# Optimization experiments

Measured on AMD Instinct MI355X. Metric: run time of the kernel, lower is better.

The kernel has to match this reference:

```python
import jax, jax.numpy as jnp
import numpy as np

HEADS = 8
DIM_HEAD = 64
CHUNK = 64        # seq chunk size
CCS = 128         # context chunk size
ALPHA = 32.0 ** 2 # stable-softmax alpha


def setup_inputs() -> dict:
    key = jax.random.key(0)
    ks = jax.random.split(key, 8)
    B, S, L, D = 4, 4097, 8065, 1024
    inner = HEADS * DIM_HEAD
    return dict(
        seq=jax.random.normal(ks[0], (B, S, D), jnp.float32),
        context=jax.random.normal(ks[1], (B, L, D), jnp.float32),
        Wq=jax.random.normal(ks[2], (D, inner), jnp.float32) * 0.02,
        Wkv=jax.random.normal(ks[3], (D, 2 * inner), jnp.float32) * 0.02,
        Wout=jax.random.normal(ks[4], (inner, D), jnp.float32) * 0.02,
        b_out=jnp.zeros((D,), jnp.float32),
        null_k=jax.random.normal(ks[5], (HEADS, DIM_HEAD), jnp.float32),
        null_v=jax.random.normal(ks[6], (HEADS, DIM_HEAD), jnp.float32),
        W_th=jax.random.normal(ks[7], (HEADS, HEADS), jnp.float32) * 0.2,
        b_th=jnp.zeros((HEADS,), jnp.float32),
    )


def reference(seq, context, Wq, Wkv, Wout, b_out, null_k, null_v, W_th, b_th):
    B, S, D = seq.shape
    # strip start tokens / pad to chunk multiples (matches torch F.pad logic)
    seq_len = S - 1                     # has_start_token -> seq_left_pad = -1
    ctx_len = context.shape[1] - 1      # context_has_start_token
    seq_rpad = (-seq_len) % CHUNK
    ctx_lpad = CCS - 1                  # context_left_pad = ccs - 1
    ctx_rpad = (-ctx_len) % CCS
    s = jnp.pad(seq[:, 1:], ((0, 0), (0, seq_rpad), (0, 0)))
    c = jnp.pad(context, ((0, 0), (ctx_lpad, ctx_rpad), (0, 0)))
    n = min(s.shape[1] // CHUNK, c.shape[1] // CCS)  # truncate to common chunks
    s = s[:, : n * CHUNK].reshape(B, n, CHUNK, D)
    c = c[:, : n * CCS].reshape(B, n, CCS, D)
    # projections -> b h n c d
    q = jnp.einsum('bncd,de->bnce', s, Wq)
    q = q.reshape(B, n, CHUNK, HEADS, DIM_HEAD).transpose(0, 3, 1, 2, 4)
    kv = jnp.einsum('bncd,de->bnce', c, Wkv)
    k, v = jnp.split(kv, 2, axis=-1)
    k = k.reshape(B, n, CCS, HEADS, DIM_HEAD).transpose(0, 3, 1, 2, 4)
    v = v.reshape(B, n, CCS, HEADS, DIM_HEAD).transpose(0, 3, 1, 2, 4)
    q = q * (DIM_HEAD ** -0.5)
    # prepend null k/v token per chunk
    nk = jnp.broadcast_to(null_k[None, :, None, None, :], (B, HEADS, n, 1, DIM_HEAD))
    nv = jnp.broadcast_to(null_v[None, :, None, None, :], (B, HEADS, n, 1, DIM_HEAD))
    k = jnp.concatenate([nk, k], axis=-2)  # [B,H,n,CCS+1,dh]
    v = jnp.concatenate([nv, v], axis=-2)
    sim = jnp.einsum('bhnid,bhnjd->bhnij', q, k)
    # stable softmax: t/alpha, subtract detached max, re-scale, softmax
    t = sim / ALPHA
    t = t - jax.lax.stop_gradient(jnp.max(t, axis=-1, keepdims=True))
    attn = jax.nn.softmax(t * ALPHA, axis=-1)
    # talking heads: 1x1x1 Conv3d over head channels
    attn = jnp.einsum('gh,bhnij->bgnij', W_th, attn) + b_th[None, :, None, None, None]
    out = jnp.einsum('bhnij,bhnjd->bhnid', attn, v)
    out = out.transpose(0, 2, 3, 1, 4).reshape(B, n * CHUNK, HEADS * DIM_HEAD)
    out = out @ Wout + b_out
    # re-insert start-token slot and pad/truncate back to original seq length
    right = (S - 1) - out.shape[1]
    out = jnp.pad(out, ((0, 0), (1, max(right, 0)), (0, 0)))
    if right < 0:
        out = out[:, :S]
    return out
```

## Files before the change

kernel.cpp:

```cpp
#include <hip/hip_runtime.h>


typedef __attribute__((ext_vector_type(8))) short bf16x8;
typedef __attribute__((ext_vector_type(4))) float f32x4;

__device__ __forceinline__ short f2bf(float x) {
  union { float f; unsigned u; } v; v.f = x;
  unsigned r = v.u + 0x7FFFu + ((v.u >> 16) & 1u);
  return (short)(r >> 16);
}
__device__ __forceinline__ short f2bf_r(float x) {
  union { float f; unsigned u; } v; v.f = x;
  return (short)((v.u + 0x8000u) >> 16);
}
__device__ __forceinline__ float bf2f(short s) {
  union { unsigned u; float f; } v;
  v.u = ((unsigned)(unsigned short)s) << 16;
  return v.f;
}

__global__ void transpose_w(const float* __restrict__ Wq, const float* __restrict__ Wkv,
                            const float* __restrict__ Wout,
                            short* __restrict__ wqT, short* __restrict__ wkvT,
                            short* __restrict__ woutT) {
  int idx = blockIdx.x * 256 + threadIdx.x;
  if (idx < 524288) {
    int d = idx >> 9, e = idx & 511;
    wqT[e * 1024 + d] = f2bf(Wq[idx]);
  } else if (idx < 1572864) {
    int i = idx - 524288;
    int d = i >> 10, e = i & 1023;
    wkvT[e * 1024 + d] = f2bf(Wkv[i]);
  } else if (idx < 2097152) {
    int i = idx - 1572864;
    int k = i >> 10, e = i & 1023;
    woutT[e * 512 + k] = f2bf(Wout[i]);
  }
}

__global__ void zero_rows(float* __restrict__ out) {
  int idx = blockIdx.x * 256 + threadIdx.x;
  if (idx < 4096) out[(size_t)(idx >> 10) * (4097u * 1024u) + (idx & 1023)] = 0.f;
}

template <int MODE>
__global__ __launch_bounds__(256, 2) void gemm_k(const void* __restrict__ Av,
                                                 const short* __restrict__ BT,
                                                 const float* __restrict__ bias,
                                                 void* __restrict__ C1v,
                                                 short* __restrict__ C2) {
  constexpr int Ksz = (MODE == 2) ? 512 : 1024;
  __shared__ short As[128 * 40];
  __shared__ short Bs[128 * 40];
  const int t = threadIdx.x;
  const int bm = blockIdx.x, bn = blockIdx.y;
  const int wid = t >> 6, lane = t & 63, qd = lane >> 4, ln = lane & 15;
  const int wm = wid >> 1, wn = wid & 1;

  const f32x4 zf = {0.f, 0.f, 0.f, 0.f};
  f32x4 acc[4][4];
#pragma unroll
  for (int it = 0; it < 4; ++it)
#pragma unroll
    for (int jt = 0; jt < 4; ++jt) acc[it][jt] = zf;

  const int arow = t >> 1;
  const int koff = (t & 1) * 16;
  const float* asrcF = nullptr;
  const short* asrcB = nullptr;
  bool avalid = true;
  {
    int gr = bm * 128 + arow;
    if constexpr (MODE == 0) {
      int b = gr >> 12, i = gr & 4095;
      asrcF = (const float*)Av + ((size_t)b * 4097 + 1 + i) * 1024;
    } else if constexpr (MODE == 1) {
      int b = gr >> 13, j = gr & 8191;
      avalid = (j >= 127);
      asrcF = (const float*)Av + ((size_t)b * 8065 + (j - 127)) * 1024;
    } else {
      asrcB = (const short*)Av + (size_t)gr * 512;
    }
  }
  const short* bsrc = BT + (size_t)(bn * 128 + arow) * Ksz;

  for (int kt = 0; kt < Ksz / 32; ++kt) {
    const int k0 = kt * 32 + koff;
    bf16x8 a0, a1;
    if constexpr (MODE == 2) {
      a0 = *(const bf16x8*)(asrcB + k0);
      a1 = *(const bf16x8*)(asrcB + k0 + 8);
    } else {
      f32x4 f0 = zf, f1 = zf, f2 = zf, f3 = zf;
      if (avalid) {
        f0 = *(const f32x4*)(asrcF + k0);
        f1 = *(const f32x4*)(asrcF + k0 + 4);
        f2 = *(const f32x4*)(asrcF + k0 + 8);
        f3 = *(const f32x4*)(asrcF + k0 + 12);
      }
#pragma unroll
      for (int i = 0; i < 4; ++i) {
        a0[i]     = f2bf_r(f0[i]);
        a0[i + 4] = f2bf_r(f1[i]);
        a1[i]     = f2bf_r(f2[i]);
        a1[i + 4] = f2bf_r(f3[i]);
      }
    }
    bf16x8 b0 = *(const bf16x8*)(bsrc + k0);
    bf16x8 b1 = *(const bf16x8*)(bsrc + k0 + 8);
    *(bf16x8*)&As[arow * 40 + koff] = a0;
    *(bf16x8*)&As[arow * 40 + koff + 8] = a1;
    *(bf16x8*)&Bs[arow * 40 + koff] = b0;
    *(bf16x8*)&Bs[arow * 40 + koff + 8] = b1;
    __syncthreads();
    bf16x8 af[4], bfv[4];
#pragma unroll
    for (int it = 0; it < 4; ++it)
      af[it] = *(const bf16x8*)&As[(wm * 64 + it * 16 + ln) * 40 + qd * 8];
#pragma unroll
    for (int jt = 0; jt < 4; ++jt)
      bfv[jt] = *(const bf16x8*)&Bs[(wn * 64 + jt * 16 + ln) * 40 + qd * 8];
#pragma unroll
    for (int it = 0; it < 4; ++it)
#pragma unroll
      for (int jt = 0; jt < 4; ++jt)
        acc[it][jt] = __builtin_amdgcn_mfma_f32_16x16x32_bf16(af[it], bfv[jt], acc[it][jt], 0, 0, 0);
    __syncthreads();
  }

#pragma unroll
  for (int it = 0; it < 4; ++it) {
    const int rbase = bm * 128 + wm * 64 + it * 16 + qd * 4;
#pragma unroll
    for (int jt = 0; jt < 4; ++jt) {
      const int cc = bn * 128 + wn * 64 + jt * 16 + ln;
      float bia = 0.f;
      if constexpr (MODE == 2) bia = bias[cc];
#pragma unroll
      for (int rr = 0; rr < 4; ++rr) {
        const int rg = rbase + rr;
        const float v = acc[it][jt][rr];
        if constexpr (MODE == 0) {
          int b = rg >> 12, i = rg & 4095;
          int nch = i >> 6, ic = i & 63;
          int h = cc >> 6, d = cc & 63;
          ((short*)C1v)[(((size_t)(b * 8 + h) * 64 + nch) * 64 + ic) * 64 + d] = f2bf(v * 0.125f);
        } else if constexpr (MODE == 1) {
          int b = rg >> 13, j = rg & 8191;
          int nch = j >> 7, jc = j & 127;
          int d = cc & 63;
          if (cc < 512) {
            int h = cc >> 6;
            ((short*)C1v)[(((size_t)(b * 8 + h) * 64 + nch) * 128 + jc) * 64 + d] = f2bf(v);
          } else {
            int h = (cc - 512) >> 6;
            C2[(((size_t)(b * 8 + h) * 64 + nch) * 128 + jc) * 64 + d] = f2bf(v);
          }
        } else {
          int b = rg >> 12, i = rg & 4095;
          ((float*)C1v)[((size_t)b * 4097 + 1 + i) * 1024 + cc] = v + bia;
        }
      }
    }
  }
}

__global__ __launch_bounds__(512, 2) void attn_kernel(
    const short* __restrict__ qws, const short* __restrict__ kws,
    const short* __restrict__ vws, const float* __restrict__ null_k,
    const float* __restrict__ null_v, const float* __restrict__ W_th,
    const float* __restrict__ b_th, short* __restrict__ ows) {
  __shared__ short P[8 * 16 * 152];

  const int blk = blockIdx.x;
  const int b = blk >> 8;
  const int rem = blk & 255;
  const int nch = rem >> 2;
  const int qh = rem & 3;
  const int tid = threadIdx.x;
  const int wid = tid >> 6;
  const int lane = tid & 63;
  const int qd = lane >> 4, ln = lane & 15;

  const bf16x8 z8 = {0, 0, 0, 0, 0, 0, 0, 0};
  const f32x4 zf = {0.f, 0.f, 0.f, 0.f};

  const short* qb = qws + ((size_t)(b * 8 + wid) * 64 + nch) * 64 * 64;
  const short* kb = kws + ((size_t)(b * 8 + wid) * 64 + nch) * 128 * 64;

  bf16x8 qf[2];
#pragma unroll
  for (int kk = 0; kk < 2; ++kk)
    qf[kk] = *(const bf16x8*)(qb + (qh * 16 + ln) * 64 + kk * 32 + qd * 8);

  f32x4 acc[9];
#pragma unroll
  for (int jt = 0; jt < 9; ++jt) acc[jt] = zf;

#pragma unroll
  for (int jt = 0; jt < 8; ++jt) {
#pragma unroll
    for (int kk = 0; kk < 2; ++kk) {
      bf16x8 bfr = *(const bf16x8*)(kb + (jt * 16 + ln) * 64 + kk * 32 + qd * 8);
      acc[jt] = __builtin_amdgcn_mfma_f32_16x16x32_bf16(qf[kk], bfr, acc[jt], 0, 0, 0);
    }
  }
  {
#pragma unroll
    for (int kk = 0; kk < 2; ++kk) {
      bf16x8 nk = z8;
      if (ln == 0) {
#pragma unroll
        for (int j = 0; j < 8; ++j)
          nk[j] = f2bf(null_k[wid * 64 + kk * 32 + qd * 8 + j]);
      }
      acc[8] = __builtin_amdgcn_mfma_f32_16x16x32_bf16(qf[kk], nk, acc[8], 0, 0, 0);
    }
  }

#pragma unroll
  for (int rr = 0; rr < 4; ++rr) {
    float v[9];
    float m = -3.0e38f;
#pragma unroll
    for (int jt = 0; jt < 9; ++jt) {
      float x = acc[jt][rr];
      if (jt == 8 && ln != 0) x = -3.0e38f;
      v[jt] = x;
      m = fmaxf(m, x);
    }
#pragma unroll
    for (int s = 1; s < 16; s <<= 1) m = fmaxf(m, __shfl_xor(m, s, 64));
    float sum = 0.f;
#pragma unroll
    for (int jt = 0; jt < 9; ++jt) {
      float e = (jt == 8 && ln != 0) ? 0.f : exp2f((v[jt] - m) * 1.44269504f);
      v[jt] = e;
      sum += e;
    }
#pragma unroll
    for (int s = 1; s < 16; s <<= 1) sum += __shfl_xor(sum, s, 64);
    const float inv = 1.0f / sum;
    const int row = qd * 4 + rr;
#pragma unroll
    for (int jt = 0; jt < 9; ++jt)
      P[(wid * 16 + row) * 152 + jt * 16 + ln] = f2bf(v[jt] * inv);
  }
  __syncthreads();

  {
    float w[64];
#pragma unroll
    for (int i = 0; i < 64; ++i) {
      union { float f; int i; } u;
      u.f = W_th[i];
      u.i = __builtin_amdgcn_readfirstlane(u.i);
      w[i] = u.f;
    }
    float bt[8];
#pragma unroll
    for (int g = 0; g < 8; ++g) {
      union { float f; int i; } u;
      u.f = b_th[g];
      u.i = __builtin_amdgcn_readfirstlane(u.i);
      bt[g] = u.f;
    }
    const int r = tid >> 5;
    const int c0 = (tid & 31) * 5;
    for (int c = c0; c < c0 + 5 && c < 129; ++c) {
      float v[8];
#pragma unroll
      for (int h = 0; h < 8; ++h) v[h] = bf2f(P[(h * 16 + r) * 152 + c]);
      float o[8];
#pragma unroll
      for (int g = 0; g < 8; ++g) {
        float s = bt[g];
#pragma unroll
        for (int h = 0; h < 8; ++h) s += w[g * 8 + h] * v[h];
        o[g] = s;
      }
#pragma unroll
      for (int g = 0; g < 8; ++g) P[(g * 16 + r) * 152 + c] = f2bf(o[g]);
    }
  }
  __syncthreads();

  const short* vb = vws + ((size_t)(b * 8 + wid) * 64 + nch) * 128 * 64;
  bf16x8 vf[4][4];
#pragma unroll
  for (int kk = 0; kk < 4; ++kk)
#pragma unroll
    for (int dt = 0; dt < 4; ++dt) {
      bf16x8 tmp;
#pragma unroll
      for (int jj = 0; jj < 8; ++jj)
        tmp[jj] = vb[(kk * 32 + qd * 8 + jj) * 64 + dt * 16 + ln];
      vf[kk][dt] = tmp;
    }

  f32x4 oacc[4];
#pragma unroll
  for (int dt = 0; dt < 4; ++dt) oacc[dt] = zf;

#pragma unroll
  for (int kk = 0; kk < 4; ++kk) {
    bf16x8 af = *(const bf16x8*)&P[(wid * 16 + ln) * 152 + kk * 32 + qd * 8];
#pragma unroll
    for (int dt = 0; dt < 4; ++dt)
      oacc[dt] = __builtin_amdgcn_mfma_f32_16x16x32_bf16(af, vf[kk][dt], oacc[dt], 0, 0, 0);
  }
  {
    float nv[4];
#pragma unroll
    for (int dt = 0; dt < 4; ++dt) nv[dt] = null_v[wid * 64 + dt * 16 + ln];
#pragma unroll
    for (int rr = 0; rr < 4; ++rr) {
      float p = bf2f(P[(wid * 16 + qd * 4 + rr) * 152 + 128]);
#pragma unroll
      for (int dt = 0; dt < 4; ++dt) oacc[dt][rr] += p * nv[dt];
    }
  }
  const size_t rowbase = (size_t)b * 4096 + nch * 64 + qh * 16;
#pragma unroll
  for (int dt = 0; dt < 4; ++dt)
#pragma unroll
    for (int rr = 0; rr < 4; ++rr)
      ows[(rowbase + qd * 4 + rr) * 512 + wid * 64 + dt * 16 + ln] = f2bf(oacc[dt][rr]);
}

extern "C" void kernel_launch(void* const* d_in, const int* in_sizes, int n_in,
                              void* d_out, int out_size, void* d_ws, size_t ws_size,
                              hipStream_t stream) {
  const float* seq   = (const float*)d_in[0];
  const float* ctx   = (const float*)d_in[1];
  const float* Wq    = (const float*)d_in[2];
  const float* Wkv   = (const float*)d_in[3];
  const float* Wout  = (const float*)d_in[4];
  const float* b_out = (const float*)d_in[5];
  const float* nullk = (const float*)d_in[6];
  const float* nullv = (const float*)d_in[7];
  const float* W_th  = (const float*)d_in[8];
  const float* b_th  = (const float*)d_in[9];

  char* ws = (char*)d_ws;
  short* qws   = (short*)(ws);
  short* kws   = (short*)(ws + 16777216);
  short* vws   = (short*)(ws + 50331648);
  short* ows   = (short*)(ws + 83886080);
  short* wqT   = (short*)(ws + 100663296);
  short* wkvT  = (short*)(ws + 101711872);
  short* woutT = (short*)(ws + 103809024);
  float* out   = (float*)d_out;

  hipLaunchKernelGGL(transpose_w, dim3(8192), dim3(256), 0, stream,
                     Wq, Wkv, Wout, wqT, wkvT, woutT);
  hipLaunchKernelGGL((gemm_k<0>), dim3(128, 4), dim3(256), 0, stream,
                     (const void*)seq, wqT, (const float*)nullptr, (void*)qws, (short*)nullptr);
  hipLaunchKernelGGL((gemm_k<1>), dim3(256, 8), dim3(256), 0, stream,
                     (const void*)ctx, wkvT, (const float*)nullptr, (void*)kws, vws);
  hipLaunchKernelGGL(attn_kernel, dim3(1024), dim3(512), 0, stream,
                     qws, kws, vws, nullk, nullv, W_th, b_th, ows);
  hipLaunchKernelGGL(zero_rows, dim3(16), dim3(256), 0, stream, out);
  hipLaunchKernelGGL((gemm_k<2>), dim3(128, 8), dim3(256), 0, stream,
                     (const void*)ows, woutT, b_out, (void*)out, (short*)nullptr);
}
```

Baseline: 520.3 us.

## Pre-convert activations to bf16 and load GEMM tiles via global_load_lds

Adds separate kernels that convert seq and padded context to bf16 buffers up front. A new GEMM variant then streams A and B tiles straight into LDS with the global-to-LDS load builtin, using an unpadded 32-wide LDS stride. The aim is to take fp32 loading and conversion out of the GEMM inner loop and cut register-path traffic. In exchange it adds an extra pass over the activations, needs more workspace, and may cause LDS bank conflicts without padding. A size check on the workspace picks the new path and falls back to the old one otherwise.

After: 514.1 us. No clear change (-1.2%).

```diff
diff --git a/kernel.cpp b/kernel.cpp
--- a/kernel.cpp
+++ b/kernel.cpp
@@ -17,6 +17,11 @@
   union { unsigned u; float f; } v;
   v.u = ((unsigned)(unsigned short)s) << 16;
   return v.f;
+}
+__device__ __forceinline__ void glds16(const short* g, short* l) {
+  __builtin_amdgcn_global_load_lds(
+      (const __attribute__((address_space(1))) void*)g,
+      (__attribute__((address_space(3))) void*)l, 16, 0, 0);
 }
 
 __global__ void transpose_w(const float* __restrict__ Wq, const float* __restrict__ Wkv,
@@ -38,20 +43,50 @@
   }
 }
 
+__global__ void conv_seq(const float* __restrict__ seq, short* __restrict__ seqb) {
+  size_t e = ((size_t)blockIdx.x * 256 + threadIdx.x) * 8;
+  int b = (int)(e >> 22);
+  int i = (int)((e >> 10) & 4095);
+  int k = (int)(e & 1023);
+  const float* src = seq + ((size_t)b * 4097 + 1 + i) * 1024 + k;
+  f32x4 f0 = *(const f32x4*)src;
+  f32x4 f1 = *(const f32x4*)(src + 4);
+  bf16x8 o;
+#pragma unroll
+  for (int j = 0; j < 4; ++j) { o[j] = f2bf_r(f0[j]); o[j + 4] = f2bf_r(f1[j]); }
+  *(bf16x8*)(seqb + e) = o;
+}
+
+__global__ void conv_ctx(const float* __restrict__ ctx, short* __restrict__ ctxb) {
+  size_t e = ((size_t)blockIdx.x * 256 + threadIdx.x) * 8;
+  int b = (int)(e >> 23);
+  int r = (int)((e >> 10) & 8191);
+  int k = (int)(e & 1023);
+  bf16x8 o = {0, 0, 0, 0, 0, 0, 0, 0};
+  if (r >= 127) {
+    const float* src = ctx + ((size_t)b * 8065 + (r - 127)) * 1024 + k;
+    f32x4 f0 = *(const f32x4*)src;
+    f32x4 f1 = *(const f32x4*)(src + 4);
+#pragma unroll
+    for (int j = 0; j < 4; ++j) { o[j] = f2bf_r(f0[j]); o[j + 4] = f2bf_r(f1[j]); }
+  }
+  *(bf16x8*)(ctxb + e) = o;
+}
+
 __global__ void zero_rows(float* __restrict__ out) {
   int idx = blockIdx.x * 256 + threadIdx.x;
   if (idx < 4096) out[(size_t)(idx >> 10) * (4097u * 1024u) + (idx & 1023)] = 0.f;
 }
 
 template <int MODE>
-__global__ __launch_bounds__(256, 2) void gemm_k(const void* __restrict__ Av,
-                                                 const short* __restrict__ BT,
-                                                 const float* __restrict__ bias,
-                                                 void* __restrict__ C1v,
-                                                 short* __restrict__ C2) {
+__global__ __launch_bounds__(256, 2) void gemm_fast(const short* __restrict__ A,
+                                                    const short* __restrict__ BT,
+                                                    const float* __restrict__ bias,
+                                                    void* __restrict__ C1v,
+                                                    short* __restrict__ C2) {
   constexpr int Ksz = (MODE == 2) ? 512 : 1024;
-  __shared__ short As[128 * 40];
-  __shared__ short Bs[128 * 40];
+  __shared__ short As[128 * 32];
+  __shared__ short Bs[128 * 32];
   const int t = threadIdx.x;
   const int bm = blockIdx.x, bn = blockIdx.y;
   const int wid = t >> 6, lane = t & 63, qd = lane >> 4, ln = lane & 15;
@@ -64,62 +99,31 @@
 #pragma unroll
     for (int jt = 0; jt < 4; ++jt) acc[it][jt] = zf;
 
-  const int arow = t >> 1;
-  const int koff = (t & 1) * 16;
-  const float* asrcF = nullptr;
-  const short* asrcB = nullptr;
-  bool avalid = true;
-  {
-    int gr = bm * 128 + arow;
-    if constexpr (MODE == 0) {
-      int b = gr >> 12, i = gr & 4095;
-      asrcF = (const float*)Av + ((size_t)b * 4097 + 1 + i) * 1024;
-    } else if constexpr (MODE == 1) {
-      int b = gr >> 13, j = gr & 8191;
-      avalid = (j >= 127);
-      asrcF = (const float*)Av + ((size_t)b * 8065 + (j - 127)) * 1024;
-    } else {
-      asrcB = (const short*)Av + (size_t)gr * 512;
-    }
-  }
-  const short* bsrc = BT + (size_t)(bn * 128 + arow) * Ksz;
+  const int srow = wid * 16 + (lane >> 2);
+  const int scol = (lane & 3) * 8;
+  const short* aA0 = A + ((size_t)bm * 128 + srow) * Ksz + scol;
+  const short* aA1 = aA0 + (size_t)64 * Ksz;
+  const short* aB0 = BT + ((size_t)bn * 128 + srow) * Ksz + scol;
+  const short* aB1 = aB0 + (size_t)64 * Ksz;
+  short* lA0 = &As[srow * 32 + scol];
+  short* lA1 = &As[(64 + srow) * 32 + scol];
+  short* lB0 = &Bs[srow * 32 + scol];
+  short* lB1 = &Bs[(64 + srow) * 32 + scol];
 
   for (int kt = 0; kt < Ksz / 32; ++kt) {
-    const int k0 = kt * 32 + koff;
-    bf16x8 a0, a1;
-    if constexpr (MODE == 2) {
-      a0 = *(const bf16x8*)(asrcB + k0);
-      a1 = *(const bf16x8*)(asrcB + k0 + 8);
-    } else {
-      f32x4 f0 = zf, f1 = zf, f2 = zf, f3 = zf;
-      if (avalid) {
-        f0 = *(const f32x4*)(asrcF + k0);
-        f1 = *(const f32x4*)(asrcF + k0 + 4);
-        f2 = *(const f32x4*)(asrcF + k0 + 8);
-        f3 = *(const f32x4*)(asrcF + k0 + 12);
-      }
-#pragma unroll
-      for (int i = 0; i < 4; ++i) {
-        a0[i]     = f2bf_r(f0[i]);
-        a0[i + 4] = f2bf_r(f1[i]);
-        a1[i]     = f2bf_r(f2[i]);
-        a1[i + 4] = f2bf_r(f3[i]);
-      }
-    }
-    bf16x8 b0 = *(const bf16x8*)(bsrc + k0);
-    bf16x8 b1 = *(const bf16x8*)(bsrc + k0 + 8);
-    *(bf16x8*)&As[arow * 40 + koff] = a0;
-    *(bf16x8*)&As[arow * 40 + koff + 8] = a1;
-    *(bf16x8*)&Bs[arow * 40 + koff] = b0;
-    *(bf16x8*)&Bs[arow * 40 + koff + 8] = b1;
+    const int ko = kt * 32;
+    glds16(aA0 + ko, lA0);
+    glds16(aA1 + ko, lA1);
+    glds16(aB0 + ko, lB0);
+    glds16(aB1 + ko, lB1);
     __syncthreads();
     bf16x8 af[4], bfv[4];
 #pragma unroll
     for (int it = 0; it < 4; ++it)
-      af[it] = *(const bf16x8*)&As[(wm * 64 + it * 16 + ln) * 40 + qd * 8];
+      af[it] = *(const bf16x8*)&As[(wm * 64 + it * 16 + ln) * 32 + qd * 8];
 #pragma unroll
     for (int jt = 0; jt < 4; ++jt)
-      bfv[jt] = *(const bf16x8*)&Bs[(wn * 64 + jt * 16 + ln) * 40 + qd * 8];
+      bfv[jt] = *(const bf16x8*)&Bs[(wn * 64 + jt * 16 + ln) * 32 + qd * 8];
 #pragma unroll
     for (int it = 0; it < 4; ++it)
 #pragma unroll
@@ -165,6 +169,128 @@
   }
 }
 
+template <int MODE>
+__global__ __launch_bounds__(256, 2) void gemm_k(const void* __restrict__ Av,
+                                                 const short* __restrict__ BT,
+                                                 const float* __restrict__ bias,
+                                                 void* __restrict__ C1v,
+                                                 short* __restrict__ C2) {
+  constexpr int Ksz = (MODE == 2) ? 512 : 1024;
+  __shared__ short As[128 * 40];
+  __shared__ short Bs[128 * 40];
+  const int t = threadIdx.x;
+  const int bm = blockIdx.x, bn = blockIdx.y;
+  const int wid = t >> 6, lane = t & 63, qd = lane >> 4, ln = lane & 15;
+  const int wm = wid >> 1, wn = wid & 1;
+
+  const f32x4 zf = {0.f, 0.f, 0.f, 0.f};
+  f32x4 acc[4][4];
+#pragma unroll
+  for (int it = 0; it < 4; ++it)
+#pragma unroll
+    for (int jt = 0; jt < 4; ++jt) acc[it][jt] = zf;
+
+  const int arow = t >> 1;
+  const int koff = (t & 1) * 16;
+  const float* asrcF = nullptr;
+  const short* asrcB = nullptr;
+  bool avalid = true;
+  {
+    int gr = bm * 128 + arow;
+    if constexpr (MODE == 0) {
+      int b = gr >> 12, i = gr & 4095;
+      asrcF = (const float*)Av + ((size_t)b * 4097 + 1 + i) * 1024;
+    } else if constexpr (MODE == 1) {
+      int b = gr >> 13, j = gr & 8191;
+      avalid = (j >= 127);
+      asrcF = (const float*)Av + ((size_t)b * 8065 + (j - 127)) * 1024;
+    } else {
+      asrcB = (const short*)Av + (size_t)gr * 512;
+    }
+  }
+  const short* bsrc = BT + (size_t)(bn * 128 + arow) * Ksz;
+
+  for (int kt = 0; kt < Ksz / 32; ++kt) {
+    const int k0 = kt * 32 + koff;
+    bf16x8 a0, a1;
+    if constexpr (MODE == 2) {
+      a0 = *(const bf16x8*)(asrcB + k0);
+      a1 = *(const bf16x8*)(asrcB + k0 + 8);
+    } else {
+      f32x4 f0 = zf, f1 = zf, f2 = zf, f3 = zf;
+      if (avalid) {
+        f0 = *(const f32x4*)(asrcF + k0);
+        f1 = *(const f32x4*)(asrcF + k0 + 4);
+        f2 = *(const f32x4*)(asrcF + k0 + 8);
+        f3 = *(const f32x4*)(asrcF + k0 + 12);
+      }
+#pragma unroll
+      for (int i = 0; i < 4; ++i) {
+        a0[i]     = f2bf_r(f0[i]);
+        a0[i + 4] = f2bf_r(f1[i]);
+        a1[i]     = f2bf_r(f2[i]);
+        a1[i + 4] = f2bf_r(f3[i]);
+      }
+    }
+    bf16x8 b0 = *(const bf16x8*)(bsrc + k0);
+    bf16x8 b1 = *(const bf16x8*)(bsrc + k0 + 8);
+    *(bf16x8*)&As[arow * 40 + koff] = a0;
+    *(bf16x8*)&As[arow * 40 + koff + 8] = a1;
+    *(bf16x8*)&Bs[arow * 40 + koff] = b0;
+    *(bf16x8*)&Bs[arow * 40 + koff + 8] = b1;
+    __syncthreads();
+    bf16x8 af[4], bfv[4];
+#pragma unroll
+    for (int it = 0; it < 4; ++it)
+      af[it] = *(const bf16x8*)&As[(wm * 64 + it * 16 + ln) * 40 + qd * 8];
+#pragma unroll
+    for (int jt = 0; jt < 4; ++jt)
+      bfv[jt] = *(const bf16x8*)&Bs[(wn * 64 + jt * 16 + ln) * 40 + qd * 8];
+#pragma unroll
+    for (int it = 0; it < 4; ++it)
+#pragma unroll
+      for (int jt = 0; jt < 4; ++jt)
+        acc[it][jt] = __builtin_amdgcn_mfma_f32_16x16x32_bf16(af[it], bfv[jt], acc[it][jt], 0, 0, 0);
+    __syncthreads();
+  }
+
+#pragma unroll
+  for (int it = 0; it < 4; ++it) {
+    const int rbase = bm * 128 + wm * 64 + it * 16 + qd * 4;
+#pragma unroll
+    for (int jt = 0; jt < 4; ++jt) {
+      const int cc = bn * 128 + wn * 64 + jt * 16 + ln;
+      float bia = 0.f;
+      if constexpr (MODE == 2) bia = bias[cc];
+#pragma unroll
+      for (int rr = 0; rr < 4; ++rr) {
+        const int rg = rbase + rr;
+        const float v = acc[it][jt][rr];
+        if constexpr (MODE == 0) {
+          int b = rg >> 12, i = rg & 4095;
+          int nch = i >> 6, ic = i & 63;
+          int h = cc >> 6, d = cc & 63;
+          ((short*)C1v)[(((size_t)(b * 8 + h) * 64 + nch) * 64 + ic) * 64 + d] = f2bf(v * 0.125f);
+        } else if constexpr (MODE == 1) {
+          int b = rg >> 13, j = rg & 8191;
+          int nch = j >> 7, jc = j & 127;
+          int d = cc & 63;
+          if (cc < 512) {
+            int h = cc >> 6;
+            ((short*)C1v)[(((size_t)(b * 8 + h) * 64 + nch) * 128 + jc) * 64 + d] = f2bf(v);
+          } else {
+            int h = (cc - 512) >> 6;
+            C2[(((size_t)(b * 8 + h) * 64 + nch) * 128 + jc) * 64 + d] = f2bf(v);
+          }
+        } else {
+          int b = rg >> 12, i = rg & 4095;
+          ((float*)C1v)[((size_t)b * 4097 + 1 + i) * 1024 + cc] = v + bia;
+        }
+      }
+    }
+  }
+}
+
 __global__ __launch_bounds__(512, 2) void attn_kernel(
     const short* __restrict__ qws, const short* __restrict__ kws,
     const short* __restrict__ vws, const float* __restrict__ null_k,
@@ -343,24 +469,52 @@
   const float* b_th  = (const float*)d_in[9];
 
   char* ws = (char*)d_ws;
-  short* qws   = (short*)(ws);
-  short* kws   = (short*)(ws + 16777216);
-  short* vws   = (short*)(ws + 50331648);
-  short* ows   = (short*)(ws + 83886080);
-  short* wqT   = (short*)(ws + 100663296);
-  short* wkvT  = (short*)(ws + 101711872);
-  short* woutT = (short*)(ws + 103809024);
-  float* out   = (float*)d_out;
-
-  hipLaunchKernelGGL(transpose_w, dim3(8192), dim3(256), 0, stream,
-                     Wq, Wkv, Wout, wqT, wkvT, woutT);
-  hipLaunchKernelGGL((gemm_k<0>), dim3(128, 4), dim3(256), 0, stream,
-                     (const void*)seq, wqT, (const float*)nullptr, (void*)qws, (short*)nullptr);
-  hipLaunchKernelGGL((gemm_k<1>), dim3(256, 8), dim3(256), 0, stream,
-                     (const void*)ctx, wkvT, (const float*)nullptr, (void*)kws, vws);
-  hipLaunchKernelGGL(attn_kernel, dim3(1024), dim3(512), 0, stream,
-                     qws, kws, vws, nullk, nullv, W_th, b_th, ows);
-  hipLaunchKernelGGL(zero_rows, dim3(16), dim3(256), 0, stream, out);
-  hipLaunchKernelGGL((gemm_k<2>), dim3(128, 8), dim3(256), 0, stream,
-                     (const void*)ows, woutT, b_out, (void*)out, (short*)nullptr);
-}
+  float* out = (float*)d_out;
+  const bool fast = ws_size >= 188743680ull;
+
+  if (fast) {
+    short* seqb  = (short*)(ws);
+    short* ows   = (short*)(ws);
+    short* ctxb  = (short*)(ws + 33554432);
+    short* qws   = (short*)(ws + 100663296);
+    short* kws   = (short*)(ws + 117440512);
+    short* vws   = (short*)(ws + 150994944);
+    short* wqT   = (short*)(ws + 184549376);
+    short* wkvT  = (short*)(ws + 185597952);
+    short* woutT = (short*)(ws + 187695104);
+
+    hipLaunchKernelGGL(transpose_w, dim3(8192), dim3(256), 0, stream,
+                       Wq, Wkv, Wout, wqT, wkvT, woutT);
+    hipLaunchKernelGGL(conv_seq, dim3(8192), dim3(256), 0, stream, seq, seqb);
+    hipLaunchKernelGGL(conv_ctx, dim3(16384), dim3(256), 0, stream, ctx, ctxb);
+    hipLaunchKernelGGL((gemm_fast<0>), dim3(128, 4), dim3(256), 0, stream,
+                       seqb, wqT, (const float*)nullptr, (void*)qws, (short*)nullptr);
+    hipLaunchKernelGGL((gemm_fast<1>), dim3(256, 8), dim3(256), 0, stream,
+                       ctxb, wkvT, (const float*)nullptr, (void*)kws, vws);
+    hipLaunchKernelGGL(attn_kernel, dim3(1024), dim3(512), 0, stream,
+                       qws, kws, vws, nullk, nullv, W_th, b_th, ows);
+    hipLaunchKernelGGL(zero_rows, dim3(16), dim3(256), 0, stream, out);
+    hipLaunchKernelGGL((gemm_fast<2>), dim3(128, 8), dim3(256), 0, stream,
+                       ows, woutT, b_out, (void*)out, (short*)nullptr);
+  } else {
+    short* qws   = (short*)(ws);
+    short* kws   = (short*)(ws + 16777216);
+    short* vws   = (short*)(ws + 50331648);
+    short* ows   = (short*)(ws + 83886080);
+    short* wqT   = (short*)(ws + 100663296);
+    short* wkvT  = (short*)(ws + 101711872);
+    short* woutT = (short*)(ws + 103809024);
+
+    hipLaunchKernelGGL(transpose_w, dim3(8192), dim3(256), 0, stream,
+                       Wq, Wkv, Wout, wqT, wkvT, woutT);
+    hipLaunchKernelGGL((gemm_k<0>), dim3(128, 4), dim3(256), 0, stream,
+                       (const void*)seq, wqT, (const float*)nullptr, (void*)qws, (short*)nullptr);
+    hipLaunchKernelGGL((gemm_k<1>), dim3(256, 8), dim3(256), 0, stream,
+                       (const void*)ctx, wkvT, (const float*)nullptr, (void*)kws, vws);
+    hipLaunchKernelGGL(attn_kernel, dim3(1024), dim3(512), 0, stream,
+                       qws, kws, vws, nullk, nullv, W_th, b_th, ows);
+    hipLaunchKernelGGL(zero_rows, dim3(16), dim3(256), 0, stream, out);
+    hipLaunchKernelGGL((gemm_k<2>), dim3(128, 8), dim3(256), 0, stream,
+                       (const void*)ows, woutT, b_out, (void*)out, (short*)nullptr);
+  }
+}
```
